# Kernel optimization log

Hardware: AMD Instinct MI355X
Metric: run time of the kernel (lower is better)

Reference implementation:

```python
import jax, jax.numpy as jnp
import numpy as np

B, S, D = 2, 2048, 1024
H, HD = 16, 64          # n_heads, head_dim
FF, HID = 4096, 8192    # d_ff, swiglu hidden (= 2*d_ff)


def _ln(x, eps=1e-5):
    # non-parametric LayerNorm (fp8_layernorm_noparam in source)
    m = jnp.mean(x, axis=-1, keepdims=True)
    v = jnp.var(x, axis=-1, keepdims=True)
    return (x - m) * jax.lax.rsqrt(v + eps)


def setup_inputs() -> dict:
    key = jax.random.key(0)
    ks = jax.random.split(key, 7)
    s = 0.02  # init std
    return {
        "x": jax.random.normal(ks[0], (B, S, D), jnp.float32),
        "Wq": jax.random.normal(ks[1], (D, D), jnp.float32) * s,
        "Wk": jax.random.normal(ks[2], (D, D), jnp.float32) * s,
        "Wv": jax.random.normal(ks[3], (D, D), jnp.float32) * s,
        "Wo": jax.random.normal(ks[4], (D, D), jnp.float32) * s,
        "Wff": jax.random.normal(ks[5], (HID, D), jnp.float32) * s,
        "Wout": jax.random.normal(ks[6], (FF, D), jnp.float32).T * s,  # [D, FF] -> stored as Linear weight [D_out=D, D_in=FF]
    }


def reference(x, Wq, Wk, Wv, Wo, Wff, Wout):
    b, s, d = x.shape
    # attention sub-block
    h = _ln(x)
    q = (h @ Wq.T).reshape(b, s, H, HD).transpose(0, 2, 1, 3)  # [B,H,S,HD]
    k = (h @ Wk.T).reshape(b, s, H, HD).transpose(0, 2, 1, 3)
    v = (h @ Wv.T).reshape(b, s, H, HD).transpose(0, 2, 1, 3)
    scale = 1.0 / float(HD) ** 0.5
    scores = jnp.einsum('bhqd,bhkd->bhqk', q, k) * scale        # [B,H,S,S] naive full matrix
    causal = jnp.tril(jnp.ones((s, s), dtype=bool))
    scores = jnp.where(causal, scores, jnp.finfo(scores.dtype).min)
    attn = jax.nn.softmax(scores, axis=-1)
    att = jnp.einsum('bhqk,bhkd->bhqd', attn, v)                # [B,H,S,HD]
    att = att.transpose(0, 2, 1, 3).reshape(b, s, d)
    x = x + att @ Wo.T
    # MLP sub-block (SwiGLU, OLMo Llama-style)
    h2 = _ln(x)
    ff = h2 @ Wff.T                                             # [B,S,HID]
    x1, x2 = jnp.split(ff, 2, axis=-1)
    g = jax.nn.silu(x1) * x2                                    # [B,S,FF]
    return x + g @ Wout.T
```

## Files before the change

kernel.cpp:

```cpp
#include <hip/hip_runtime.h>
#include <hip/hip_bf16.h>

#define B_ 2
#define S_ 2048
#define D_ 1024
#define H_ 16
#define FF_ 4096
#define M_ (B_*S_)

using u16 = unsigned short;
using u32 = unsigned int;
typedef __attribute__((ext_vector_type(8))) short short8;
typedef __attribute__((ext_vector_type(4))) float f32x4;
typedef __attribute__((ext_vector_type(16))) float f32x16;
typedef __attribute__((ext_vector_type(4))) unsigned short u16x4;
typedef __attribute__((ext_vector_type(4))) unsigned int u32x4;

static __device__ __forceinline__ u16 f2bf(float f) {
  __hip_bfloat16 h = __float2bfloat16(f);
  return *reinterpret_cast<u16*>(&h);
}
static __device__ __forceinline__ float bf2f(u16 u) {
  __hip_bfloat16 h; *reinterpret_cast<u16*>(&h) = u;
  return __bfloat162float(h);
}

#define GLDS(gp, lp) __builtin_amdgcn_global_load_lds( \
    (const __attribute__((address_space(1))) void*)(gp), \
    (__attribute__((address_space(3))) void*)(lp), 16, 0, 0)

#define MFMA16(a, b, c) __builtin_amdgcn_mfma_f32_16x16x32_bf16(a, b, c, 0, 0, 0)
#define VMC(n) asm volatile("s_waitcnt vmcnt(" #n ")" ::: "memory")
#define BAR() __builtin_amdgcn_s_barrier()
#define CFENCE() asm volatile("" ::: "memory")

static __device__ __forceinline__ void tile_decode(
    int lin, int nwg, int gridN, int& bm, int& bn) {
  lin = (lin & 7) * (nwg >> 3) + (lin >> 3);
  int st = lin >> 6, u = lin & 63;
  int nstx = gridN >> 3;
  bm = (st / nstx) * 8 + (u >> 3);
  bn = (st % nstx) * 8 + (u & 7);
}

__global__ __launch_bounds__(256) void conv_all(
    const float* __restrict__ Wq, const float* __restrict__ Wk,
    const float* __restrict__ Wv, const float* __restrict__ Wo,
    const float* __restrict__ Wff, const float* __restrict__ Wout,
    u16* __restrict__ wqkv, u16* __restrict__ wo,
    u16* __restrict__ wff, u16* __restrict__ wout) {
  int bid = blockIdx.x;
  const float* src; u16* dst; int off;
  if (bid < 1024)       { src = Wq;   dst = wqkv;           off = bid; }
  else if (bid < 2048)  { src = Wk;   dst = wqkv + 1048576; off = bid - 1024; }
  else if (bid < 3072)  { src = Wv;   dst = wqkv + 2097152; off = bid - 2048; }
  else if (bid < 4096)  { src = Wo;   dst = wo;             off = bid - 3072; }
  else if (bid < 12288) { src = Wff;  dst = wff;            off = bid - 4096; }
  else                  { src = Wout; dst = wout;           off = bid - 12288; }
  int i = off * 256 + threadIdx.x;
  float4 v = reinterpret_cast<const float4*>(src)[i];
  u16x4 o;
  o.x = f2bf(v.x); o.y = f2bf(v.y); o.z = f2bf(v.z); o.w = f2bf(v.w);
  reinterpret_cast<u16x4*>(dst)[i] = o;
}

__global__ __launch_bounds__(256) void ln_rows(
    const float* __restrict__ x, u16* __restrict__ out) {
  int row = blockIdx.x;
  int t = threadIdx.x;
  float4 v = reinterpret_cast<const float4*>(x + (size_t)row * D_)[t];
  float s  = v.x + v.y + v.z + v.w;
  float ss = v.x*v.x + v.y*v.y + v.z*v.z + v.w*v.w;
  #pragma unroll
  for (int off = 1; off < 64; off <<= 1) {
    s  += __shfl_xor(s,  off, 64);
    ss += __shfl_xor(ss, off, 64);
  }
  __shared__ float rs[4], rss[4];
  int wid = t >> 6;
  if ((t & 63) == 0) { rs[wid] = s; rss[wid] = ss; }
  __syncthreads();
  s  = rs[0] + rs[1] + rs[2] + rs[3];
  ss = rss[0] + rss[1] + rss[2] + rss[3];
  float mean = s * (1.0f / D_);
  float var  = ss * (1.0f / D_) - mean * mean;
  float r = rsqrtf(var + 1e-5f);
  u16x4 o;
  o.x = f2bf((v.x - mean) * r);
  o.y = f2bf((v.y - mean) * r);
  o.z = f2bf((v.z - mean) * r);
  o.w = f2bf((v.w - mean) * r);
  reinterpret_cast<u16x4*>(out + (size_t)row * D_)[t] = o;
}

template<int MODE>
__global__ __launch_bounds__(256, 2) void gemm_bt2(
    const u16* __restrict__ A, const u16* __restrict__ W,
    void* __restrict__ C, const float* __restrict__ res, int M, int N, int K)
{
  __shared__ u16 lds[32768];
  const int tid = threadIdx.x;
  const int wid = tid >> 6, lane = tid & 63;
  const int g = lane >> 4, c = lane & 15;
  const int gridN = N >> 7;
  int bm, bn;
  tile_decode(blockIdx.x, gridDim.x, gridN, bm, bn);
  const int wm = wid >> 1, wn = wid & 1;
  const int NT = K >> 6;

  f32x4 acc[4][4];
  #pragma unroll
  for (int i = 0; i < 4; i++)
    #pragma unroll
    for (int j = 0; j < 4; j++) acc[i][j] = {0.f, 0.f, 0.f, 0.f};

  auto stage = [&](int sel, int t) {
    const u16* src = sel ? W : A;
    const int tilerow = (sel ? bn : bm) * 128;
    char* dst = (char*)&lds[sel * 16384 + (t & 1) * 8192];
    #pragma unroll
    for (int i = 0; i < 4; i++) {
      int j = i * 256 + tid;
      int row = j >> 3, col16 = j & 7;
      const u16* gp = src + (size_t)(tilerow + row) * K + t * 64 + ((col16 ^ (row & 7)) << 3);
      GLDS(gp, dst + j * 16);
    }
  };

  stage(0, 0); stage(1, 0);
  __syncthreads();

  for (int t = 0; t < NT; t++) {
    const int buf = t & 1;
    if (t + 1 < NT) { stage(0, t + 1); stage(1, t + 1); }

    short8 af[2][4], bfr[2][4];
    #pragma unroll
    for (int ks = 0; ks < 2; ks++)
      #pragma unroll
      for (int m = 0; m < 4; m++) {
        int rh = wm * 64 + m * 16 + c;
        af[ks][m] = *reinterpret_cast<const short8*>(
            &lds[buf * 8192 + rh * 64 + ((((ks << 2) | g) ^ (rh & 7)) << 3)]);
      }
    #pragma unroll
    for (int ks = 0; ks < 2; ks++)
      #pragma unroll
      for (int n = 0; n < 4; n++) {
        int rh = wn * 64 + n * 16 + c;
        bfr[ks][n] = *reinterpret_cast<const short8*>(
            &lds[16384 + buf * 8192 + rh * 64 + ((((ks << 2) | g) ^ (rh & 7)) << 3)]);
      }
    __builtin_amdgcn_s_setprio(1);
    #pragma unroll
    for (int m = 0; m < 4; m++)
      #pragma unroll
      for (int n = 0; n < 4; n++) {
        acc[m][n] = MFMA16(af[0][m], bfr[0][n], acc[m][n]);
        acc[m][n] = MFMA16(af[1][m], bfr[1][n], acc[m][n]);
      }
    __builtin_amdgcn_s_setprio(0);
    __syncthreads();
  }

  #pragma unroll
  for (int m = 0; m < 4; m++)
    #pragma unroll
    for (int n = 0; n < 4; n++)
      #pragma unroll
      for (int r = 0; r < 4; r++) {
        int gr = bm * 128 + wm * 64 + m * 16 + g * 4 + r;
        int gc = bn * 128 + wn * 64 + n * 16 + c;
        size_t idx = (size_t)gr * N + gc;
        float v = acc[m][n][r];
        if (MODE == 0) {
          ((u16*)C)[idx] = f2bf(v);
        } else {
          ((float*)C)[idx] = v + res[idx];
        }
      }
}

__global__ __launch_bounds__(256, 2) void gemm_ff(
    const u16* __restrict__ A, const u16* __restrict__ W,
    u16* __restrict__ Cout, int M, int N, int K)
{
  __shared__ u16 lds[36864];
  const int tid = threadIdx.x;
  const int wid = tid >> 6, lane = tid & 63;
  const int g = lane >> 4, c = lane & 15;
  const int gridN = N >> 7;
  int bm, bn;
  tile_decode(blockIdx.x, gridDim.x, gridN, bm, bn);
  const int wm = wid >> 1, wn = wid & 1;
  const int NT = K >> 5;

  f32x4 ac1[4][4], ac2[4][4];
  #pragma unroll
  for (int i = 0; i < 4; i++)
    #pragma unroll
    for (int j = 0; j < 4; j++) { ac1[i][j] = {0.f,0.f,0.f,0.f}; ac2[i][j] = {0.f,0.f,0.f,0.f}; }

  auto stage = [&](int t) {
    #pragma unroll
    for (int sel = 0; sel < 3; sel++) {
      const u16* src = (sel == 0) ? A : W;
      const int rowbase = (sel == 0) ? bm * 128 : (sel == 1 ? bn * 128 : 4096 + bn * 128);
      char* dst = (char*)&lds[sel * 12288 + (t % 3) * 4096];
      #pragma unroll
      for (int i = 0; i < 2; i++) {
        int j = i * 256 + tid;
        int r = j >> 2, cslot = j & 3;
        const u16* gp = src + (size_t)(rowbase + r) * K + t * 32 + ((cslot ^ ((r >> 1) & 3)) * 8);
        GLDS(gp, dst + j * 16);
      }
    }
  };

  stage(0); stage(1);

  for (int t = 0; t < NT; t++) {
    if (t + 1 < NT) { VMC(6); } else { VMC(0); }
    BAR(); CFENCE();
    if (t + 2 < NT) stage(t + 2);

    const int buf = t % 3;
    short8 af[4], b1f[4], b2f[4];
    #pragma unroll
    for (int m = 0; m < 4; m++) {
      int rh = wm * 64 + m * 16 + c;
      af[m] = *reinterpret_cast<const short8*>(
          &lds[buf * 4096 + rh * 32 + ((g ^ ((rh >> 1) & 3)) << 3)]);
    }
    #pragma unroll
    for (int n = 0; n < 4; n++) {
      int rh = wn * 64 + n * 16 + c;
      b1f[n] = *reinterpret_cast<const short8*>(
          &lds[12288 + buf * 4096 + rh * 32 + ((g ^ ((rh >> 1) & 3)) << 3)]);
      b2f[n] = *reinterpret_cast<const short8*>(
          &lds[24576 + buf * 4096 + rh * 32 + ((g ^ ((rh >> 1) & 3)) << 3)]);
    }
    __builtin_amdgcn_s_setprio(1);
    #pragma unroll
    for (int m = 0; m < 4; m++)
      #pragma unroll
      for (int n = 0; n < 4; n++) {
        ac1[m][n] = MFMA16(af[m], b1f[n], ac1[m][n]);
        ac2[m][n] = MFMA16(af[m], b2f[n], ac2[m][n]);
      }
    __builtin_amdgcn_s_setprio(0);
  }

  #pragma unroll
  for (int m = 0; m < 4; m++)
    #pragma unroll
    for (int n = 0; n < 4; n++)
      #pragma unroll
      for (int r = 0; r < 4; r++) {
        int gr = bm * 128 + wm * 64 + m * 16 + g * 4 + r;
        int gc = bn * 128 + wn * 64 + n * 16 + c;
        float v1 = ac1[m][n][r];
        float v2 = ac2[m][n][r];
        float gv = (v1 / (1.0f + __expf(-v1))) * v2;
        Cout[(size_t)gr * N + gc] = f2bf(gv);
      }
}

__global__ __launch_bounds__(256) void transpose_v(
    const u16* __restrict__ qkv, u16* __restrict__ vT) {
  __shared__ u16 t[64][66];
  int bh = blockIdx.y;
  int s0 = blockIdx.x * 64;
  int b = bh >> 4, h = bh & 15;
  int tid = threadIdx.x;
  #pragma unroll
  for (int it = 0; it < 2; it++) {
    int idx = it * 256 + tid;
    int row = idx >> 3;
    int cc  = (idx & 7) * 8;
    const u16* src = qkv + ((size_t)(b * S_ + s0 + row)) * 3072 + 2048 + h * 64 + cc;
    short8 v = *reinterpret_cast<const short8*>(src);
    #pragma unroll
    for (int j = 0; j < 8; j++) t[row][cc + j] = (u16)v[j];
  }
  __syncthreads();
  #pragma unroll
  for (int it = 0; it < 2; it++) {
    int idx = it * 256 + tid;
    int d  = idx >> 3;
    int sc = (idx & 7) * 8;
    short8 o;
    #pragma unroll
    for (int j = 0; j < 8; j++) o[j] = (short)t[sc + j][d];
    *reinterpret_cast<short8*>(vT + ((size_t)bh * 64 + d) * S_ + s0 + sc) = o;
  }
}

__global__ __launch_bounds__(256) void attn_split(
    const u16* __restrict__ qkv, const u16* __restrict__ vT,
    u16* __restrict__ pO, float* __restrict__ pML, u16* __restrict__ att) {
  __shared__ u16 Kl[3][2048];
  __shared__ u16 Vl[3][2048];
  const int tid  = threadIdx.x;
  const int lane = tid & 63;
  const int wid  = tid >> 6;
  const int l31  = lane & 31;
  const int half = lane >> 5;

  int lin = blockIdx.x;
  int swz = (lin & 7) * 160 + (lin >> 3);
  int bh  = swz / 40;
  int j   = swz - bh * 40;
  int qq = 15, rem = j;
  while (rem > (qq >> 2)) { rem -= (qq >> 2) + 1; qq--; }
  int ci = rem;
  const int qt  = qq * 4 + wid;
  const int kt0 = ci * 16;
  const int nt  = min(qq * 4 + 3, kt0 + 15) - kt0;
  int ubase = (qt < 16) ? qt : (qt < 32) ? 16 + (qt - 16) * 2 + ci
            : (qt < 48) ? 48 + (qt - 32) * 3 + ci : 96 + (qt - 48) * 4 + ci;
  const int punit = bh * 160 + ubase;

  const int b = bh >> 4, hd = bh & 15;
  const int q_base = qt * 32;

  const u16* Qb = qkv + ((size_t)(b * S_ + q_base + l31)) * 3072 + hd * 64;
  const u16* Kb = qkv + (size_t)b * S_ * 3072 + 1024 + hd * 64;
  const u16* Vt = vT + (size_t)bh * 64 * S_;

  short8 qf[4];
  #pragma unroll
  for (int dt = 0; dt < 4; dt++) {
    short8 v = *reinterpret_cast<const short8*>(Qb + dt * 16 + half * 8);
    #pragma unroll
    for (int jj = 0; jj < 8; jj++) v[jj] = (short)f2bf(bf2f((u16)v[jj]) * 0.18033688f);
    qf[dt] = v;
  }

  auto stageKV = [&](int kt, int buf) {
    {
      int row = tid >> 3, cs = tid & 7;
      int c = cs ^ (row & 7);
      const u16* gp = Kb + (size_t)(kt * 32 + row) * 3072 + c * 8;
      GLDS(gp, (char*)&Kl[buf][0] + tid * 16);
    }
    {
      int row = tid >> 2, cs = tid & 3;
      int c = cs ^ ((row >> 1) & 3);
      const u16* gp = Vt + (size_t)row * S_ + kt * 32 + c * 8;
      GLDS(gp, (char*)&Vl[buf][0] + tid * 16);
    }
  };

  f32x16 o0, o1;
  #pragma unroll
  for (int r = 0; r < 16; r++) { o0[r] = 0.f; o1[r] = 0.f; }
  float lsum = 0.f;

  stageKV(kt0, 0);
  if (nt >= 1) { stageKV(kt0 + 1, 1); VMC(2); } else { VMC(0); }
  BAR();

  for (int i = 0; ; i++) {
    const int kt = kt0 + i;
    const int buf = i % 3;
    if (i + 2 <= nt) stageKV(kt0 + i + 2, (i + 2) % 3);

    if (kt <= qt) {
      const bool diag = (kt == qt);
      short8 kfr[4], vfr[4];
      #pragma unroll
      for (int dt = 0; dt < 4; dt++) {
        int cs = (dt * 2 + half) ^ (l31 & 7);
        kfr[dt] = *reinterpret_cast<const short8*>((const char*)&Kl[buf][0] + l31 * 128 + cs * 16);
      }
      {
        int r0 = l31, r1 = 32 + l31;
        int x0 = (r0 >> 1) & 3, x1 = (r1 >> 1) & 3;
        vfr[0] = *reinterpret_cast<const short8*>((const char*)&Vl[buf][0] + r0 * 64 + ((half       ^ x0) * 16));
        vfr[1] = *reinterpret_cast<const short8*>((const char*)&Vl[buf][0] + r0 * 64 + (((2 + half) ^ x0) * 16));
        vfr[2] = *reinterpret_cast<const short8*>((const char*)&Vl[buf][0] + r1 * 64 + ((half       ^ x1) * 16));
        vfr[3] = *reinterpret_cast<const short8*>((const char*)&Vl[buf][0] + r1 * 64 + (((2 + half) ^ x1) * 16));
      }

      f32x16 s;
      #pragma unroll
      for (int r = 0; r < 16; r++) s[r] = 0.f;
      __builtin_amdgcn_s_setprio(1);
      #pragma unroll
      for (int dt = 0; dt < 4; dt++)
        s = __builtin_amdgcn_mfma_f32_32x32x16_bf16(kfr[dt], qf[dt], s, 0, 0, 0);
      __builtin_amdgcn_s_setprio(0);

      float p[16];
      float rs = 0.f;
      #pragma unroll
      for (int r = 0; r < 16; r++) {
        float pv = exp2f(s[r]);
        if (diag) {
          int kloc = half * 4 + (r & 3) + 8 * (r >> 2);
          if (kloc > l31) pv = 0.f;
        }
        p[r] = pv;
        rs += pv;
      }
      rs += __shfl_xor(rs, 32, 64);
      lsum += rs;

      u32 pk[8], sp[8];
      #pragma unroll
      for (int ii = 0; ii < 8; ii++) {
        pk[ii] = (u32)f2bf(p[2 * ii]) | ((u32)f2bf(p[2 * ii + 1]) << 16);
        sp[ii] = (u32)__shfl_xor((int)pk[ii], 32, 64);
      }
      u32x4 a0 = { half ? sp[2] : pk[0], half ? sp[3] : pk[1],
                   half ? pk[2] : sp[0], half ? pk[3] : sp[1] };
      u32x4 a1 = { half ? sp[6] : pk[4], half ? sp[7] : pk[5],
                   half ? pk[6] : sp[4], half ? pk[7] : sp[5] };
      short8 pa0 = *reinterpret_cast<short8*>(&a0);
      short8 pa1 = *reinterpret_cast<short8*>(&a1);

      __builtin_amdgcn_s_setprio(1);
      o0 = __builtin_amdgcn_mfma_f32_32x32x16_bf16(pa0, vfr[0], o0, 0, 0, 0);
      o0 = __builtin_amdgcn_mfma_f32_32x32x16_bf16(pa1, vfr[1], o0, 0, 0, 0);
      o1 = __builtin_amdgcn_mfma_f32_32x32x16_bf16(pa0, vfr[2], o1, 0, 0, 0);
      o1 = __builtin_amdgcn_mfma_f32_32x32x16_bf16(pa1, vfr[3], o1, 0, 0, 0);
      __builtin_amdgcn_s_setprio(0);
    }

    if (i == nt) break;
    if (i + 2 <= nt) { VMC(2); } else { VMC(0); }
    BAR();
  }

  if (qt < 16) {
    #pragma unroll
    for (int r = 0; r < 16; r++) {
      int row = (r & 3) + 8 * (r >> 2) + 4 * half;
      float inv = 1.0f / __shfl(lsum, row, 64);
      size_t base = ((size_t)(b * S_ + q_base + row)) * D_ + hd * 64 + l31;
      att[base]      = f2bf(o0[r] * inv);
      att[base + 32] = f2bf(o1[r] * inv);
    }
  } else {
    #pragma unroll
    for (int r = 0; r < 16; r++) {
      int row = (r & 3) + 8 * (r >> 2) + 4 * half;
      pO[(size_t)punit * 2048 + row * 64 + l31]      = f2bf(o0[r]);
      pO[(size_t)punit * 2048 + row * 64 + 32 + l31] = f2bf(o1[r]);
    }
    if (half == 0) pML[punit * 32 + l31] = lsum;
  }
}

__global__ __launch_bounds__(256) void attn_combine(
    const u16* __restrict__ pO, const float* __restrict__ pML,
    u16* __restrict__ att) {
  int gw = blockIdx.x;
  int bh = gw / 48, qt = 16 + gw % 48;
  int b = bh >> 4, hd = bh & 15;
  int nc = (qt >> 4) + 1;
  int base = (qt < 32) ? 16 + (qt - 16) * 2
           : (qt < 48) ? 48 + (qt - 32) * 3 : 96 + (qt - 48) * 4;
  int p0 = bh * 160 + base;
  int q  = threadIdx.x >> 3;
  int d  = (threadIdx.x & 7) * 8;

  float L = pML[p0 * 32 + q] + pML[(p0 + 1) * 32 + q];
  if (nc > 2) L += pML[(p0 + 2) * 32 + q];
  if (nc > 3) L += pML[(p0 + 3) * 32 + q];
  float invL = 1.0f / L;

  float o[8];
  short8 v0 = *reinterpret_cast<const short8*>(&pO[(size_t)p0 * 2048 + q * 64 + d]);
  short8 v1 = *reinterpret_cast<const short8*>(&pO[(size_t)(p0 + 1) * 2048 + q * 64 + d]);
  #pragma unroll
  for (int jj = 0; jj < 8; jj++) o[jj] = bf2f((u16)v0[jj]) + bf2f((u16)v1[jj]);
  if (nc > 2) {
    short8 v = *reinterpret_cast<const short8*>(&pO[(size_t)(p0 + 2) * 2048 + q * 64 + d]);
    #pragma unroll
    for (int jj = 0; jj < 8; jj++) o[jj] += bf2f((u16)v[jj]);
  }
  if (nc > 3) {
    short8 v = *reinterpret_cast<const short8*>(&pO[(size_t)(p0 + 3) * 2048 + q * 64 + d]);
    #pragma unroll
    for (int jj = 0; jj < 8; jj++) o[jj] += bf2f((u16)v[jj]);
  }
  short8 ov;
  #pragma unroll
  for (int jj = 0; jj < 8; jj++) ov[jj] = (short)f2bf(o[jj] * invL);
  *reinterpret_cast<short8*>(
      &att[((size_t)(b * S_ + qt * 32 + q)) * D_ + hd * 64 + d]) = ov;
}

extern "C" void kernel_launch(void* const* d_in, const int* in_sizes, int n_in,
                              void* d_out, int out_size, void* d_ws, size_t ws_size,
                              hipStream_t stream) {
  (void)in_sizes; (void)n_in; (void)out_size; (void)ws_size;
  const float* x    = (const float*)d_in[0];
  const float* Wq   = (const float*)d_in[1];
  const float* Wk   = (const float*)d_in[2];
  const float* Wv   = (const float*)d_in[3];
  const float* Wo   = (const float*)d_in[4];
  const float* Wff  = (const float*)d_in[5];
  const float* Wout = (const float*)d_in[6];
  float* out = (float*)d_out;

  char* ws = (char*)d_ws;
  u16*   wqkv = (u16*)(ws);
  u16*   wo   = (u16*)(ws + 6291456);
  u16*   wff  = (u16*)(ws + 8388608);
  u16*   wout = (u16*)(ws + 25165824);
  float* x1   = (float*)(ws + 33554432);
  char*  P    = ws + 50331648;
  u16*   hbuf = (u16*)(P);
  u16*   qkv  = (u16*)(P + 8388608);
  u16*   vT   = (u16*)(P + 33554432);
  u16*   att  = (u16*)(P + 41943040);
  u16*   pO   = (u16*)(P + 50331648);
  float* pML  = (float*)(P + 71303168);
  u16*   h2   = (u16*)(P);
  u16*   gbuf = (u16*)(P + 41943040);

  conv_all<<<16384, 256, 0, stream>>>(Wq, Wk, Wv, Wo, Wff, Wout,
                                      wqkv, wo, wff, wout);

  ln_rows<<<M_, 256, 0, stream>>>(x, hbuf);
  gemm_bt2<0><<<dim3(768), 256, 0, stream>>>(hbuf, wqkv, qkv, nullptr, M_, 3072, 1024);
  transpose_v<<<dim3(32, 32), 256, 0, stream>>>(qkv, vT);
  attn_split<<<dim3(1280), 256, 0, stream>>>(qkv, vT, pO, pML, att);
  attn_combine<<<dim3(1536), 256, 0, stream>>>(pO, pML, att);
  gemm_bt2<1><<<dim3(256), 256, 0, stream>>>(att, wo, x1, x, M_, 1024, 1024);

  ln_rows<<<M_, 256, 0, stream>>>(x1, h2);
  gemm_ff<<<dim3(1024), 256, 0, stream>>>(h2, wff, gbuf, M_, 4096, 1024);
  gemm_bt2<1><<<dim3(256), 256, 0, stream>>>(gbuf, wout, out, x1, M_, 1024, 4096);
}
```

Before: 258.3 us.

## Use 128x64 tiles for N=1024 GEMMs and double-buffer gemm_ff for more occupancy

Adds gemm_bt2h, a GEMM with 128x64 output tiles and K-step 64 with double-buffered LDS, used for the Wo and Wout projections. This launches 512 blocks instead of 256, so the 256 compute units get better coverage. gemm_ff drops from triple to double buffering with a full barrier per step, cutting LDS so three blocks can fit per CU. The trade is shallower prefetch and a sync every iteration, which may expose memory latency.

```diff
diff --git a/kernel.cpp b/kernel.cpp
--- a/kernel.cpp
+++ b/kernel.cpp
@@ -181,11 +181,102 @@
       }
 }
 
-__global__ __launch_bounds__(256, 2) void gemm_ff(
+template<int MODE>
+__global__ __launch_bounds__(256, 2) void gemm_bt2h(
+    const u16* __restrict__ A, const u16* __restrict__ W,
+    void* __restrict__ C, const float* __restrict__ res, int M, int N, int K)
+{
+  __shared__ u16 lds[24576];
+  const int tid = threadIdx.x;
+  const int wid = tid >> 6, lane = tid & 63;
+  const int g = lane >> 4, c = lane & 15;
+  const int gridN = N >> 6;
+  int bm, bn;
+  tile_decode(blockIdx.x, gridDim.x, gridN, bm, bn);
+  const int wm = wid >> 1, wn = wid & 1;
+  const int NT = K >> 6;
+
+  f32x4 acc[4][2];
+  #pragma unroll
+  for (int i = 0; i < 4; i++)
+    #pragma unroll
+    for (int j = 0; j < 2; j++) acc[i][j] = {0.f, 0.f, 0.f, 0.f};
+
+  auto stage = [&](int sel, int t) {
+    const u16* src = sel ? W : A;
+    const int tilerow = sel ? bn * 64 : bm * 128;
+    char* dst = sel ? (char*)&lds[16384 + (t & 1) * 4096]
+                    : (char*)&lds[(t & 1) * 8192];
+    const int nldr = sel ? 2 : 4;
+    #pragma unroll
+    for (int i = 0; i < 4; i++) {
+      if (i >= nldr) break;
+      int j = i * 256 + tid;
+      int row = j >> 3, col16 = j & 7;
+      const u16* gp = src + (size_t)(tilerow + row) * K + t * 64 + ((col16 ^ (row & 7)) << 3);
+      GLDS(gp, dst + j * 16);
+    }
+  };
+
+  stage(0, 0); stage(1, 0);
+  __syncthreads();
+
+  for (int t = 0; t < NT; t++) {
+    const int buf = t & 1;
+    if (t + 1 < NT) { stage(0, t + 1); stage(1, t + 1); }
+
+    short8 af[2][4], bfr[2][2];
+    #pragma unroll
+    for (int ks = 0; ks < 2; ks++)
+      #pragma unroll
+      for (int m = 0; m < 4; m++) {
+        int rh = wm * 64 + m * 16 + c;
+        af[ks][m] = *reinterpret_cast<const short8*>(
+            &lds[buf * 8192 + rh * 64 + ((((ks << 2) | g) ^ (rh & 7)) << 3)]);
+      }
+    #pragma unroll
+    for (int ks = 0; ks < 2; ks++)
+      #pragma unroll
+      for (int n = 0; n < 2; n++) {
+        int rh = wn * 32 + n * 16 + c;
+        bfr[ks][n] = *reinterpret_cast<const short8*>(
+            &lds[16384 + buf * 4096 + rh * 64 + ((((ks << 2) | g) ^ (rh & 7)) << 3)]);
+      }
+    __builtin_amdgcn_s_setprio(1);
+    #pragma unroll
+    for (int m = 0; m < 4; m++)
+      #pragma unroll
+      for (int n = 0; n < 2; n++) {
+        acc[m][n] = MFMA16(af[0][m], bfr[0][n], acc[m][n]);
+        acc[m][n] = MFMA16(af[1][m], bfr[1][n], acc[m][n]);
+      }
+    __builtin_amdgcn_s_setprio(0);
+    __syncthreads();
+  }
+
+  #pragma unroll
+  for (int m = 0; m < 4; m++)
+    #pragma unroll
+    for (int n = 0; n < 2; n++)
+      #pragma unroll
+      for (int r = 0; r < 4; r++) {
+        int gr = bm * 128 + wm * 64 + m * 16 + g * 4 + r;
+        int gc = bn * 64 + wn * 32 + n * 16 + c;
+        size_t idx = (size_t)gr * N + gc;
+        float v = acc[m][n][r];
+        if (MODE == 0) {
+          ((u16*)C)[idx] = f2bf(v);
+        } else {
+          ((float*)C)[idx] = v + res[idx];
+        }
+      }
+}
+
+__global__ __launch_bounds__(256, 3) void gemm_ff(
     const u16* __restrict__ A, const u16* __restrict__ W,
     u16* __restrict__ Cout, int M, int N, int K)
 {
-  __shared__ u16 lds[36864];
+  __shared__ u16 lds[24576];
   const int tid = threadIdx.x;
   const int wid = tid >> 6, lane = tid & 63;
   const int g = lane >> 4, c = lane & 15;
@@ -206,7 +297,7 @@
     for (int sel = 0; sel < 3; sel++) {
       const u16* src = (sel == 0) ? A : W;
       const int rowbase = (sel == 0) ? bm * 128 : (sel == 1 ? bn * 128 : 4096 + bn * 128);
-      char* dst = (char*)&lds[sel * 12288 + (t % 3) * 4096];
+      char* dst = (char*)&lds[sel * 8192 + (t & 1) * 4096];
       #pragma unroll
       for (int i = 0; i < 2; i++) {
         int j = i * 256 + tid;
@@ -217,14 +308,13 @@
     }
   };
 
-  stage(0); stage(1);
+  stage(0);
+  __syncthreads();
 
   for (int t = 0; t < NT; t++) {
-    if (t + 1 < NT) { VMC(6); } else { VMC(0); }
-    BAR(); CFENCE();
-    if (t + 2 < NT) stage(t + 2);
-
-    const int buf = t % 3;
+    const int buf = t & 1;
+    if (t + 1 < NT) stage(t + 1);
+
     short8 af[4], b1f[4], b2f[4];
     #pragma unroll
     for (int m = 0; m < 4; m++) {
@@ -236,9 +326,9 @@
     for (int n = 0; n < 4; n++) {
       int rh = wn * 64 + n * 16 + c;
       b1f[n] = *reinterpret_cast<const short8*>(
-          &lds[12288 + buf * 4096 + rh * 32 + ((g ^ ((rh >> 1) & 3)) << 3)]);
+          &lds[8192 + buf * 4096 + rh * 32 + ((g ^ ((rh >> 1) & 3)) << 3)]);
       b2f[n] = *reinterpret_cast<const short8*>(
-          &lds[24576 + buf * 4096 + rh * 32 + ((g ^ ((rh >> 1) & 3)) << 3)]);
+          &lds[16384 + buf * 4096 + rh * 32 + ((g ^ ((rh >> 1) & 3)) << 3)]);
     }
     __builtin_amdgcn_s_setprio(1);
     #pragma unroll
@@ -249,6 +339,7 @@
         ac2[m][n] = MFMA16(af[m], b2f[n], ac2[m][n]);
       }
     __builtin_amdgcn_s_setprio(0);
+    __syncthreads();
   }
 
   #pragma unroll
@@ -530,9 +621,9 @@
   transpose_v<<<dim3(32, 32), 256, 0, stream>>>(qkv, vT);
   attn_split<<<dim3(1280), 256, 0, stream>>>(qkv, vT, pO, pML, att);
   attn_combine<<<dim3(1536), 256, 0, stream>>>(pO, pML, att);
-  gemm_bt2<1><<<dim3(256), 256, 0, stream>>>(att, wo, x1, x, M_, 1024, 1024);
+  gemm_bt2h<1><<<dim3(512), 256, 0, stream>>>(att, wo, x1, x, M_, 1024, 1024);
 
   ln_rows<<<M_, 256, 0, stream>>>(x1, h2);
   gemm_ff<<<dim3(1024), 256, 0, stream>>>(h2, wff, gbuf, M_, 4096, 1024);
-  gemm_bt2<1><<<dim3(256), 256, 0, stream>>>(gbuf, wout, out, x1, M_, 1024, 4096);
-}
+  gemm_bt2h<1><<<dim3(512), 256, 0, stream>>>(gbuf, wout, out, x1, M_, 1024, 4096);
+}
```

New measurement: 427.5 us. +65.5%, slower.

## Fuse first LayerNorm into weight conversion and halve GEMM N-tile to 64

Applied to the files above, without the earlier changes.

Folds the first LayerNorm pass into the weight-conversion launch by appending 4096 row blocks to it, removing one kernel launch. All bt2 GEMMs switch from 128x128 to 128x64 tiles, doubling the grid (for example 256 to 512 blocks on the N=1024 projections). The goal is better CU occupancy on MI355X's many CUs. In exchange, each tile does more A-tile reloads per FLOP and has lower arithmetic intensity.

```diff
diff --git a/kernel.cpp b/kernel.cpp
--- a/kernel.cpp
+++ b/kernel.cpp
@@ -43,25 +43,54 @@
   bn = (st % nstx) * 8 + (u & 7);
 }
 
-__global__ __launch_bounds__(256) void conv_all(
+__global__ __launch_bounds__(256) void conv_ln(
     const float* __restrict__ Wq, const float* __restrict__ Wk,
     const float* __restrict__ Wv, const float* __restrict__ Wo,
     const float* __restrict__ Wff, const float* __restrict__ Wout,
     u16* __restrict__ wqkv, u16* __restrict__ wo,
-    u16* __restrict__ wff, u16* __restrict__ wout) {
+    u16* __restrict__ wff, u16* __restrict__ wout,
+    const float* __restrict__ x, u16* __restrict__ hbuf) {
   int bid = blockIdx.x;
-  const float* src; u16* dst; int off;
-  if (bid < 1024)       { src = Wq;   dst = wqkv;           off = bid; }
-  else if (bid < 2048)  { src = Wk;   dst = wqkv + 1048576; off = bid - 1024; }
-  else if (bid < 3072)  { src = Wv;   dst = wqkv + 2097152; off = bid - 2048; }
-  else if (bid < 4096)  { src = Wo;   dst = wo;             off = bid - 3072; }
-  else if (bid < 12288) { src = Wff;  dst = wff;            off = bid - 4096; }
-  else                  { src = Wout; dst = wout;           off = bid - 12288; }
-  int i = off * 256 + threadIdx.x;
-  float4 v = reinterpret_cast<const float4*>(src)[i];
-  u16x4 o;
-  o.x = f2bf(v.x); o.y = f2bf(v.y); o.z = f2bf(v.z); o.w = f2bf(v.w);
-  reinterpret_cast<u16x4*>(dst)[i] = o;
+  if (bid < 16384) {
+    const float* src; u16* dst; int off;
+    if (bid < 1024)       { src = Wq;   dst = wqkv;           off = bid; }
+    else if (bid < 2048)  { src = Wk;   dst = wqkv + 1048576; off = bid - 1024; }
+    else if (bid < 3072)  { src = Wv;   dst = wqkv + 2097152; off = bid - 2048; }
+    else if (bid < 4096)  { src = Wo;   dst = wo;             off = bid - 3072; }
+    else if (bid < 12288) { src = Wff;  dst = wff;            off = bid - 4096; }
+    else                  { src = Wout; dst = wout;           off = bid - 12288; }
+    int i = off * 256 + threadIdx.x;
+    float4 v = reinterpret_cast<const float4*>(src)[i];
+    u16x4 o;
+    o.x = f2bf(v.x); o.y = f2bf(v.y); o.z = f2bf(v.z); o.w = f2bf(v.w);
+    reinterpret_cast<u16x4*>(dst)[i] = o;
+  } else {
+    int row = bid - 16384;
+    int t = threadIdx.x;
+    float4 v = reinterpret_cast<const float4*>(x + (size_t)row * D_)[t];
+    float s  = v.x + v.y + v.z + v.w;
+    float ss = v.x*v.x + v.y*v.y + v.z*v.z + v.w*v.w;
+    #pragma unroll
+    for (int off = 1; off < 64; off <<= 1) {
+      s  += __shfl_xor(s,  off, 64);
+      ss += __shfl_xor(ss, off, 64);
+    }
+    __shared__ float rs[4], rss[4];
+    int wid = t >> 6;
+    if ((t & 63) == 0) { rs[wid] = s; rss[wid] = ss; }
+    __syncthreads();
+    s  = rs[0] + rs[1] + rs[2] + rs[3];
+    ss = rss[0] + rss[1] + rss[2] + rss[3];
+    float mean = s * (1.0f / D_);
+    float var  = ss * (1.0f / D_) - mean * mean;
+    float r = rsqrtf(var + 1e-5f);
+    u16x4 o;
+    o.x = f2bf((v.x - mean) * r);
+    o.y = f2bf((v.y - mean) * r);
+    o.z = f2bf((v.z - mean) * r);
+    o.w = f2bf((v.w - mean) * r);
+    reinterpret_cast<u16x4*>(hbuf + (size_t)row * D_)[t] = o;
+  }
 }
 
 __global__ __launch_bounds__(256) void ln_rows(
@@ -94,32 +123,35 @@
 }
 
 template<int MODE>
-__global__ __launch_bounds__(256, 2) void gemm_bt2(
+__global__ __launch_bounds__(256, 2) void gemm_bt2h(
     const u16* __restrict__ A, const u16* __restrict__ W,
     void* __restrict__ C, const float* __restrict__ res, int M, int N, int K)
 {
-  __shared__ u16 lds[32768];
+  __shared__ u16 lds[24576];
   const int tid = threadIdx.x;
   const int wid = tid >> 6, lane = tid & 63;
   const int g = lane >> 4, c = lane & 15;
-  const int gridN = N >> 7;
+  const int gridN = N >> 6;
   int bm, bn;
   tile_decode(blockIdx.x, gridDim.x, gridN, bm, bn);
   const int wm = wid >> 1, wn = wid & 1;
   const int NT = K >> 6;
 
-  f32x4 acc[4][4];
+  f32x4 acc[4][2];
   #pragma unroll
   for (int i = 0; i < 4; i++)
     #pragma unroll
-    for (int j = 0; j < 4; j++) acc[i][j] = {0.f, 0.f, 0.f, 0.f};
+    for (int j = 0; j < 2; j++) acc[i][j] = {0.f, 0.f, 0.f, 0.f};
 
   auto stage = [&](int sel, int t) {
     const u16* src = sel ? W : A;
-    const int tilerow = (sel ? bn : bm) * 128;
-    char* dst = (char*)&lds[sel * 16384 + (t & 1) * 8192];
+    const int tilerow = sel ? bn * 64 : bm * 128;
+    char* dst = sel ? (char*)&lds[16384 + (t & 1) * 4096]
+                    : (char*)&lds[(t & 1) * 8192];
+    const int nldr = sel ? 2 : 4;
     #pragma unroll
     for (int i = 0; i < 4; i++) {
+      if (i >= nldr) break;
       int j = i * 256 + tid;
       int row = j >> 3, col16 = j & 7;
       const u16* gp = src + (size_t)(tilerow + row) * K + t * 64 + ((col16 ^ (row & 7)) << 3);
@@ -134,7 +166,7 @@
     const int buf = t & 1;
     if (t + 1 < NT) { stage(0, t + 1); stage(1, t + 1); }
 
-    short8 af[2][4], bfr[2][4];
+    short8 af[2][4], bfr[2][2];
     #pragma unroll
     for (int ks = 0; ks < 2; ks++)
       #pragma unroll
@@ -146,16 +178,16 @@
     #pragma unroll
     for (int ks = 0; ks < 2; ks++)
       #pragma unroll
-      for (int n = 0; n < 4; n++) {
-        int rh = wn * 64 + n * 16 + c;
+      for (int n = 0; n < 2; n++) {
+        int rh = wn * 32 + n * 16 + c;
         bfr[ks][n] = *reinterpret_cast<const short8*>(
-            &lds[16384 + buf * 8192 + rh * 64 + ((((ks << 2) | g) ^ (rh & 7)) << 3)]);
+            &lds[16384 + buf * 4096 + rh * 64 + ((((ks << 2) | g) ^ (rh & 7)) << 3)]);
       }
     __builtin_amdgcn_s_setprio(1);
     #pragma unroll
     for (int m = 0; m < 4; m++)
       #pragma unroll
-      for (int n = 0; n < 4; n++) {
+      for (int n = 0; n < 2; n++) {
         acc[m][n] = MFMA16(af[0][m], bfr[0][n], acc[m][n]);
         acc[m][n] = MFMA16(af[1][m], bfr[1][n], acc[m][n]);
       }
@@ -166,11 +198,11 @@
   #pragma unroll
   for (int m = 0; m < 4; m++)
     #pragma unroll
-    for (int n = 0; n < 4; n++)
+    for (int n = 0; n < 2; n++)
       #pragma unroll
       for (int r = 0; r < 4; r++) {
         int gr = bm * 128 + wm * 64 + m * 16 + g * 4 + r;
-        int gc = bn * 128 + wn * 64 + n * 16 + c;
+        int gc = bn * 64 + wn * 32 + n * 16 + c;
         size_t idx = (size_t)gr * N + gc;
         float v = acc[m][n][r];
         if (MODE == 0) {
@@ -522,17 +554,16 @@
   u16*   h2   = (u16*)(P);
   u16*   gbuf = (u16*)(P + 41943040);
 
-  conv_all<<<16384, 256, 0, stream>>>(Wq, Wk, Wv, Wo, Wff, Wout,
-                                      wqkv, wo, wff, wout);
-
-  ln_rows<<<M_, 256, 0, stream>>>(x, hbuf);
-  gemm_bt2<0><<<dim3(768), 256, 0, stream>>>(hbuf, wqkv, qkv, nullptr, M_, 3072, 1024);
+  conv_ln<<<20480, 256, 0, stream>>>(Wq, Wk, Wv, Wo, Wff, Wout,
+                                     wqkv, wo, wff, wout, x, hbuf);
+
+  gemm_bt2h<0><<<dim3(1536), 256, 0, stream>>>(hbuf, wqkv, qkv, nullptr, M_, 3072, 1024);
   transpose_v<<<dim3(32, 32), 256, 0, stream>>>(qkv, vT);
   attn_split<<<dim3(1280), 256, 0, stream>>>(qkv, vT, pO, pML, att);
   attn_combine<<<dim3(1536), 256, 0, stream>>>(pO, pML, att);
-  gemm_bt2<1><<<dim3(256), 256, 0, stream>>>(att, wo, x1, x, M_, 1024, 1024);
+  gemm_bt2h<1><<<dim3(512), 256, 0, stream>>>(att, wo, x1, x, M_, 1024, 1024);
 
   ln_rows<<<M_, 256, 0, stream>>>(x1, h2);
   gemm_ff<<<dim3(1024), 256, 0, stream>>>(h2, wff, gbuf, M_, 4096, 1024);
-  gemm_bt2<1><<<dim3(256), 256, 0, stream>>>(gbuf, wout, out, x1, M_, 1024, 4096);
-}
+  gemm_bt2h<1><<<dim3(512), 256, 0, stream>>>(gbuf, wout, out, x1, M_, 1024, 4096);
+}
```

Result: no change. 255.7 us (-1.0%).
